# Kernel optimization log

Measured on AMD Instinct MI355X. Metric: run time of the kernel, lower is better.

## Reference

```python
import jax, jax.numpy as jnp
import numpy as np

EPS = 1e-6

def oneplus(x):
    return 1.0 + jnp.log1p(jnp.exp(x) + EPS)

def content_addr(mem, keys, strength):
    # mem [B,N,M], keys [B,R,M], strength [B,R] -> [B,R,N]
    mn = jnp.sqrt(jnp.sum(mem * mem, -1))    # [B,N]
    kn = jnp.sqrt(jnp.sum(keys * keys, -1))  # [B,R]
    sim = jnp.einsum('brm,bnm->brn', keys, mem) / (kn[..., None] * mn[:, None, :] + EPS)
    return jax.nn.softmax(strength[..., None] * sim, axis=-1)

def setup_inputs() -> dict:
    key = jax.random.key(0)
    ks = jax.random.split(key, 16)
    B, T, W, R, N, M = 16, 32, 128, 4, 512, 128
    def lin(k, fi, fo):
        k1, k2 = jax.random.split(k)
        s = 1.0 / np.sqrt(fi)
        return (jax.random.uniform(k1, (fi, fo), minval=-s, maxval=s),
                jax.random.uniform(k2, (fo,), minval=-s, maxval=s))
    Din = W + R * W  # controller input: cat(x_t, prev_reads)
    Wb, bb = lin(ks[0], Din + W, W)     # CfC backbone (1 layer, silu)
    Wff1, bff1 = lin(ks[1], W, W)
    Wff2, bff2 = lin(ks[2], W, W)
    Wta, bta = lin(ks[3], W, W)
    Wtb, btb = lin(ks[4], W, W)
    Wv, bv = lin(ks[5], W, W)
    Wr, br = lin(ks[6], W * R, W)
    Wxi, bxi = lin(ks[7], W, W * R + 3 * W + 5 * R + 3)
    X = jax.random.normal(ks[8], (B, T, W), dtype=jnp.float32)
    hs = jnp.zeros((B, W), dtype=jnp.float32)
    mem = jax.random.normal(ks[9], (B, N, M), dtype=jnp.float32) * 0.1
    reset_idxs = jax.random.randint(ks[10], (B, T), 0, 2, dtype=jnp.int32)
    return {'X': X, 'hs': hs, 'mem': mem, 'reset_idxs': reset_idxs,
            'Wb': Wb, 'bb': bb, 'Wff1': Wff1, 'bff1': bff1, 'Wff2': Wff2, 'bff2': bff2,
            'Wta': Wta, 'bta': bta, 'Wtb': Wtb, 'btb': btb,
            'Wv': Wv, 'bv': bv, 'Wr': Wr, 'br': br, 'Wxi': Wxi, 'bxi': bxi}

def dnc_forward(X, hs, mem, reset_idxs, Wb, bb, Wff1, bff1, Wff2, bff2,
                Wta, bta, Wtb, btb, Wv, bv, Wr, br, Wxi, bxi):
    B, T, W = X.shape
    N, M = mem.shape[1], mem.shape[2]
    R = (bxi.shape[0] - 3 * W - 3) // (W + 5)
    eye = jnp.eye(N, dtype=mem.dtype)

    def step(carry, inp):
        hs, memv, prev_reads, prev_rw, prev_ww, usage, prec, link = carry
        x_t, reset, t = inp
        r = reset.astype(x_t.dtype)
        memv = memv * (1 - r)[:, None, None]   # memory.reset_idx
        hs = hs * (1 - r)[:, None]
        # CfC controller cell
        z = jax.nn.silu(jnp.concatenate([x_t, prev_reads, hs], -1) @ Wb + bb)
        ff1 = z @ Wff1 + bff1
        ff2 = z @ Wff2 + bff2
        ti = jax.nn.sigmoid((z @ Wta + bta) * t + (z @ Wtb + btb))
        hs = ff1 * (1 - ti) + ti * ff2
        # interface vector split
        xi = hs @ Wxi + bxi
        p = 0
        read_keys = xi[:, :W * R].reshape(B, R, W); p = W * R
        write_key = xi[:, p:p + W]; p += W
        write_vec = xi[:, p:p + W]; p += W
        erase = jax.nn.sigmoid(xi[:, p:p + W]); p += W
        free_g = jax.nn.sigmoid(xi[:, p:p + R]); p += R
        read_str = oneplus(xi[:, p:p + R]); p += R
        read_modes = jax.nn.softmax(xi[:, p:p + 3 * R].reshape(B, R, 3), -1); p += 3 * R
        write_str = oneplus(xi[:, p:p + 1]); p += 1
        alloc_g = jax.nn.sigmoid(xi[:, p:p + 1]); p += 1
        write_g = jax.nn.sigmoid(xi[:, p:p + 1])
        # write weights
        wca = content_addr(memv, write_key[:, None, :], write_str)[:, 0]  # [B,N]
        retention = jnp.prod(1 - free_g[:, :, None] * prev_rw, axis=1)
        usage = (usage + prev_ww - usage * prev_ww) * retention
        si = jnp.argsort(usage, -1)
        cp = jnp.cumprod(jnp.take_along_axis(usage, si, -1), -1)
        alloc = (1 - usage) * jnp.take_along_axis(cp, si, -1)  # gather(1, sorted_idx), as in source
        ww = write_g * (alloc_g * alloc + (1 - alloc_g) * wca)  # [B,N]
        wc = ww[:, :, None]
        link = (1 - wc - jnp.swapaxes(wc, 1, 2)) * link + wc * prec[:, None, :]
        link = link * (1 - eye)
        prec = (1 - ww.sum(-1, keepdims=True)) * prec + ww
        memv = memv * (1 - wc * erase[:, None, :]) + wc * write_vec[:, None, :]
        # read
        rca = content_addr(memv, read_keys, read_str)              # [B,R,N]
        fw = jnp.einsum('brn,bnk->brk', prev_rw, link)
        bw = jnp.einsum('brn,bkn->brk', prev_rw, link)
        aux = jnp.stack([bw, rca, fw], 2)                          # [B,R,3,N]
        rw = (aux * read_modes[..., None]).sum(2)
        reads = jnp.einsum('brn,bnm->brm', rw, memv).reshape(B, R * M)
        y = hs @ Wv + bv + reads @ Wr + br
        # prev_reads is detached each step in the source
        carry = (hs, memv, jax.lax.stop_gradient(reads), rw, ww, usage, prec, link)
        return carry, (y, hs)

    dt = X.dtype
    init = (hs, mem,
            jnp.zeros((B, R * W), dt), jnp.zeros((B, R, N), dt), jnp.zeros((B, N), dt),
            jnp.zeros((B, N), dt), jnp.zeros((B, N), dt), jnp.zeros((B, N, N), dt))
    xs = (jnp.swapaxes(X, 0, 1), jnp.swapaxes(reset_idxs, 0, 1), jnp.arange(T, dtype=dt))
    _, (ys, hss) = jax.lax.scan(step, init, xs)
    return jnp.swapaxes(ys, 0, 1), jnp.swapaxes(hss, 0, 1)

def reference(X, hs, mem, reset_idxs, Wb, bb, Wff1, bff1, Wff2, bff2,
              Wta, bta, Wtb, btb, Wv, bv, Wr, br, Wxi, bxi):
    return dnc_forward(X, hs, mem, reset_idxs, Wb, bb, Wff1, bff1, Wff2, bff2,
                       Wta, bta, Wtb, btb, Wv, bv, Wr, br, Wxi, bxi)
```

## Files before the change

kernel.cpp:

```cpp
#include <hip/hip_runtime.h>
#include <math.h>

#define Bq 16
#define Tq 32
#define Wq 128
#define Rq 4
#define Nq 512
#define Mq 128
#define DINq 768
#define XIDq 919
#define BTWq (Bq*Tq*Wq)

#define TSTRIDE 31232
#define TF_FW    0
#define TF_BW    16384
#define TF_RCA   18432
#define TF_RW    20480
#define TF_PR    22528
#define TF_WC    26624
#define TF_WW    27136
#define TF_PREC  27648
#define TF_XI    28672
#define TF_CNT   29696

struct P {
  const float *X, *hs0, *mem0;
  const int *rst;
  const float *Wb,*bb,*Wff1,*bff1,*Wff2,*bff2,*Wta,*bta,*Wtb,*btb,*Wv,*bv,*Wr,*br,*Wxi,*bxi;
  float *out;
  float *rdh,*teams;
  float *WbT,*Wff1T,*Wff2T,*WtaT,*WtbT,*WvT,*WrT,*WxiT;
};

__device__ __forceinline__ float dot4(float4 a, float4 b){
  return a.x*b.x + a.y*b.y + a.z*b.z + a.w*b.w;
}
__device__ __forceinline__ float sigf(float x){ return 1.f/(1.f+expf(-x)); }
__device__ __forceinline__ float oneplusf(float x){ return 1.f + log1pf(expf(x) + 1e-6f); }

__device__ __forceinline__ void pst(float* p, float v){
  __hip_atomic_store(p, v, __ATOMIC_RELAXED, __HIP_MEMORY_SCOPE_AGENT);
}
__device__ __forceinline__ float pld(float* p){
  return __hip_atomic_load(p, __ATOMIC_RELAXED, __HIP_MEMORY_SCOPE_AGENT);
}
__device__ __forceinline__ void bump(unsigned* f){
  __syncthreads();
  if (threadIdx.x==0)
    __hip_atomic_fetch_add(f, 1u, __ATOMIC_RELAXED, __HIP_MEMORY_SCOPE_AGENT);
}
__device__ __forceinline__ void waitge(unsigned* f, unsigned v){
  if (threadIdx.x==0){
    while (__hip_atomic_fetch_add(f, 0u, __ATOMIC_RELAXED, __HIP_MEMORY_SCOPE_AGENT) < v)
      __builtin_amdgcn_s_sleep(1);
  }
  __syncthreads();
}

__device__ __forceinline__ float wave_sum64(float v){
  #pragma unroll
  for (int m=32;m>=1;m>>=1) v += __shfl_xor(v, m, 64);
  return v;
}
__device__ __forceinline__ float wave_max64(float v){
  #pragma unroll
  for (int m=32;m>=1;m>>=1) v = fmaxf(v, __shfl_xor(v, m, 64));
  return v;
}
__device__ __forceinline__ float blk_sum(float v, float* s8){
  int w = threadIdx.x>>6;
  v = wave_sum64(v);
  if ((threadIdx.x&63)==0) s8[w] = v;
  __syncthreads();
  float r = s8[0]+s8[1]+s8[2]+s8[3]+s8[4]+s8[5]+s8[6]+s8[7];
  __syncthreads();
  return r;
}
__device__ __forceinline__ float blk_max(float v, float* s8){
  int w = threadIdx.x>>6;
  v = wave_max64(v);
  if ((threadIdx.x&63)==0) s8[w] = v;
  __syncthreads();
  float r = s8[0];
  #pragma unroll
  for (int q=1;q<8;q++) r = fmaxf(r, s8[q]);
  __syncthreads();
  return r;
}

__global__ __launch_bounds__(256) void k_init(P p){
  int bid=blockIdx.x, tid=threadIdx.x;
  if (bid<8){ int idx=bid*256+tid, st=8*256;
    for (int k=idx;k<DINq*Wq;k+=st){ int j=k/DINq,i=k%DINq; p.WbT[k]=p.Wb[i*Wq+j]; }
  } else if (bid<10){ int idx=(bid-8)*256+tid, st=2*256;
    for (int k=idx;k<Wq*Wq;k+=st){ int j=k/Wq,i=k%Wq; p.Wff1T[k]=p.Wff1[i*Wq+j]; }
  } else if (bid<12){ int idx=(bid-10)*256+tid, st=2*256;
    for (int k=idx;k<Wq*Wq;k+=st){ int j=k/Wq,i=k%Wq; p.Wff2T[k]=p.Wff2[i*Wq+j]; }
  } else if (bid<14){ int idx=(bid-12)*256+tid, st=2*256;
    for (int k=idx;k<Wq*Wq;k+=st){ int j=k/Wq,i=k%Wq; p.WtaT[k]=p.Wta[i*Wq+j]; }
  } else if (bid<16){ int idx=(bid-14)*256+tid, st=2*256;
    for (int k=idx;k<Wq*Wq;k+=st){ int j=k/Wq,i=k%Wq; p.WtbT[k]=p.Wtb[i*Wq+j]; }
  } else if (bid<18){ int idx=(bid-16)*256+tid, st=2*256;
    for (int k=idx;k<Wq*Wq;k+=st){ int j=k/Wq,i=k%Wq; p.WvT[k]=p.Wv[i*Wq+j]; }
  } else if (bid<22){ int idx=(bid-18)*256+tid, st=4*256;
    for (int k=idx;k<Rq*Wq*Wq;k+=st){ int j=k/(Rq*Wq),i=k%(Rq*Wq); p.WrT[k]=p.Wr[i*Wq+j]; }
  } else if (bid<30){ int idx=(bid-22)*256+tid, st=8*256;
    for (int k=idx;k<XIDq*Wq;k+=st){ int f=k/Wq,i=k%Wq; p.WxiT[k]=p.Wxi[i*XIDq+f]; }
  } else if (bid<38){ int idx=(bid-30)*256+tid, st=8*256;
    for (int k=idx;k<16*TSTRIDE;k+=st) p.teams[k]=0.f;
  }
}

__global__ __launch_bounds__(512,2) void k_run(P p){
  const int tid=threadIdx.x, bid=blockIdx.x;
  const bool isA = (bid<16);
  const int team = isA ? bid : ((bid-16)>>3);
  const int g    = isA ? 0   : ((bid-16)&7);
  const int b=team;
  const int w=tid>>6, l=tid&63;
  float* T = p.teams + (size_t)team*TSTRIDE;
  unsigned* C = (unsigned*)(T+TF_CNT);
  unsigned* CNT_FW=C+0; unsigned* FLAG_RW=C+32; unsigned* CNT_RD=C+64;
  unsigned* FLAG_XI=C+96; unsigned* CNT_WC=C+128; unsigned* FLAG_WW=C+160;

  __shared__ __align__(16) float rwl[Rq*Nq];
  __shared__ __align__(16) float xil[XIDq+9];
  __shared__ __align__(16) float wwl[Nq];
  __shared__ __align__(16) float precl[Nq];
  __shared__ __align__(16) float usage[Nq];
  __shared__ __align__(16) float uarr[Nq];
  __shared__ __align__(16) float cpl[Nq];
  __shared__ __align__(16) int   sidx[Nq];
  __shared__ __align__(16) float wcas[Nq];
  __shared__ __align__(16) float inv[DINq];
  __shared__ __align__(16) float zl[Wq];
  __shared__ __align__(16) float hsl[Wq];
  __shared__ __align__(16) float acc4[4*Wq];
  __shared__ __align__(16) float scrA[Rq*Nq];
  __shared__ __align__(16) float scrB[Rq*Nq];
  __shared__ __align__(16) float scrC[Rq*Nq];
  __shared__ float s8[8];

  if (isA){
    for (int i=tid;i<Rq*Nq;i+=512) rwl[i]=0.f;
    usage[tid]=0.f; precl[tid]=0.f; wwl[tid]=0.f;
    if (tid<Wq) hsl[tid]=p.hs0[b*Wq+tid];
    __syncthreads();

    for (int t=0;t<=Tq;t++){
      if (t>0){
        waitge(CNT_FW, 8u*(unsigned)t);
        float* rcl=scrA; float* fwl=scrB; float* bwl=scrC;
        #pragma unroll
        for (int k=0;k<4;k++){
          int idx=tid+k*512;
          float f=0.f;
          #pragma unroll
          for (int gg=0;gg<8;gg++) f+=pld(T+TF_FW+gg*2048+idx);
          fwl[idx]=f;
          bwl[idx]=pld(T+TF_BW+idx);
          rcl[idx]=pld(T+TF_RCA+idx);
        }
        __syncthreads();
        #pragma unroll
        for (int r=0;r<Rq;r++){
          float v=rcl[r*Nq+tid];
          float mx=blk_max(v,s8);
          float e=expf(v-mx);
          float se=blk_sum(e,s8);
          rcl[r*Nq+tid]=e/se;
        }
        __syncthreads();
        #pragma unroll
        for (int k=0;k<4;k++){
          int idx=tid+k*512, r=idx>>9;
          float m0=xil[904+r*3],m1=xil[905+r*3],m2=xil[906+r*3];
          float mm=fmaxf(m0,fmaxf(m1,m2));
          float e0=expf(m0-mm),e1=expf(m1-mm),e2=expf(m2-mm);
          float es=e0+e1+e2;
          float rwv=(e0*bwl[idx]+e1*rcl[idx]+e2*fwl[idx])/es;
          rwl[idx]=rwv;
          pst(T+TF_RW+idx,rwv);
        }
      } else {
        #pragma unroll
        for (int k=0;k<4;k++){ int idx=tid+k*512; rwl[idx]=0.f; pst(T+TF_RW+idx,0.f); }
      }
      bump(FLAG_RW);
      waitge(CNT_RD, 8u*(unsigned)(t+1));
      if (t>0){
        float s=0.f;
        #pragma unroll
        for (int gg=0;gg<8;gg++) s+=pld(T+TF_PR+gg*512+tid);
        inv[Wq+tid]=s;
        p.rdh[((size_t)b*Tq+(t-1))*Nq+tid]=s;
      } else inv[Wq+tid]=0.f;
      if (t==Tq) break;
      __syncthreads();
      float keep=1.f-(float)p.rst[b*Tq+t];
      if (tid<Wq){ inv[tid]=p.X[((size_t)b*Tq+t)*Wq+tid]; inv[Wq+Nq+tid]=keep*hsl[tid]; }
      __syncthreads();
      { int j=tid>>2,q=tid&3;
        const float4* w4=(const float4*)(p.WbT+(size_t)j*DINq);
        const float4* i4=(const float4*)inv;
        float a=0.f;
        for (int c=q;c<192;c+=4) a+=dot4(w4[c],i4[c]);
        a+=__shfl_xor(a,1,4); a+=__shfl_xor(a,2,4);
        if (q==0){ a+=p.bb[j]; zl[j]=a*sigf(a); }
      }
      __syncthreads();
      { int which=tid>>7,j=tid&127;
        const float* Wg=(which==0)?p.Wff1T:(which==1)?p.Wff2T:(which==2)?p.WtaT:p.WtbT;
        const float4* w4=(const float4*)(Wg+(size_t)j*Wq);
        const float4* z4=(const float4*)zl;
        float a=0.f;
        #pragma unroll 8
        for (int c=0;c<32;c++) a+=dot4(w4[c],z4[c]);
        acc4[which*Wq+j]=a;
      }
      __syncthreads();
      if (tid<Wq){
        float a1=acc4[tid]+p.bff1[tid],a2=acc4[Wq+tid]+p.bff2[tid];
        float aa=acc4[2*Wq+tid]+p.bta[tid],ab=acc4[3*Wq+tid]+p.btb[tid];
        float ti=sigf(aa*(float)t+ab);
        float h=a1*(1.f-ti)+ti*a2;
        hsl[tid]=h;
        p.out[BTWq+((size_t)b*Tq+t)*Wq+tid]=h;
      }
      __syncthreads();
      { const float4* h4=(const float4*)hsl;
        { const float4* w4=(const float4*)(p.WxiT+(size_t)tid*Wq);
          float a=p.bxi[tid];
          #pragma unroll 8
          for (int c=0;c<32;c++) a+=dot4(w4[c],h4[c]);
          xil[tid]=a; pst(T+TF_XI+tid,a);
        }
        int f2=tid+512;
        if (f2<XIDq){
          const float4* w4=(const float4*)(p.WxiT+(size_t)f2*Wq);
          float a=p.bxi[f2];
          #pragma unroll 8
          for (int c=0;c<32;c++) a+=dot4(w4[c],h4[c]);
          xil[f2]=a; pst(T+TF_XI+f2,a);
        }
      }
      bump(FLAG_XI);
      int n=tid;
      float ret=1.f;
      #pragma unroll
      for (int r=0;r<Rq;r++) ret*=1.f-sigf(xil[896+r])*rwl[r*Nq+n];
      float uo=usage[n],pw=wwl[n];
      float u=(uo+pw-uo*pw)*ret;
      usage[n]=u; uarr[n]=u;
      __syncthreads();
      int rank=0;
      const float4* u4=(const float4*)uarr;
      #pragma unroll 8
      for (int jj=0;jj<128;jj++){
        float4 vv=u4[jj]; int j0=jj*4;
        rank+=(vv.x<u)||(vv.x==u&&(j0+0)<n);
        rank+=(vv.y<u)||(vv.y==u&&(j0+1)<n);
        rank+=(vv.z<u)||(vv.z==u&&(j0+2)<n);
        rank+=(vv.w<u)||(vv.w==u&&(j0+3)<n);
      }
      sidx[rank]=n;
      __syncthreads();
      int si=sidx[n];
      float sv=uarr[si];
      float x=sv;
      #pragma unroll
      for (int dd=1;dd<64;dd<<=1){ float pr=__shfl_up(x,dd,64); if (l>=dd) x*=pr; }
      if (l==63) s8[w]=x;
      __syncthreads();
      float woff=1.f;
      #pragma unroll
      for (int q=0;q<8;q++) if (q<w) woff*=s8[q];
      x*=woff;
      cpl[n]=x;
      waitge(CNT_WC, 8u*(unsigned)(t+1));
      { float v=pld(T+TF_WC+tid);
        float mx=blk_max(v,s8);
        float e=expf(v-mx);
        float se=blk_sum(e,s8);
        wcas[tid]=e/se;
      }
      __syncthreads();
      float alloc=(1.f-u)*cpl[si];
      float ag=sigf(xil[917]),wg=sigf(xil[918]);
      float wwv=wg*(ag*alloc+(1.f-ag)*wcas[n]);
      wwl[n]=wwv;
      pst(T+TF_WW+n,wwv);
      float wsum=blk_sum(wwv,s8);
      float pn=(1.f-wsum)*precl[n]+wwv;
      precl[n]=pn;
      pst(T+TF_PREC+(t&1)*Nq+n,pn);
      bump(FLAG_WW);
    }
  } else {
    const int rg=l>>3, cg=l&7;
    const int n_own=g*64+w*8+rg;
    const int c0=cg*16;
    float4 m4[4]; float nrm;
    { const float4* src=(const float4*)(p.mem0+((size_t)b*Nq+n_own)*Mq+c0);
      float s=0.f;
      #pragma unroll
      for (int i=0;i<4;i++){ m4[i]=src[i]; s+=dot4(m4[i],m4[i]); }
      s+=__shfl_xor(s,1,8); s+=__shfl_xor(s,2,8); s+=__shfl_xor(s,4,8);
      nrm=sqrtf(s);
    }
    float Lreg[8][8];
    #pragma unroll
    for (int rr=0;rr<8;rr++)
      #pragma unroll
      for (int q=0;q<8;q++) Lreg[rr][q]=0.f;

    for (int t=0;t<=Tq;t++){
      waitge(FLAG_RW, (unsigned)(t+1));
      for (int i=tid;i<Rq*Nq;i+=512) rwl[i]=pld(T+TF_RW+i);
      float* prl=wcas;
      prl[tid]=0.f;
      __syncthreads();
      #pragma unroll
      for (int r=0;r<Rq;r++){
        float rwn=rwl[r*Nq+n_own];
        #pragma unroll
        for (int i=0;i<4;i++){
          float ax=rwn*m4[i].x, ay=rwn*m4[i].y, az=rwn*m4[i].z, aw=rwn*m4[i].w;
          ax+=__shfl_xor(ax,8,64); ax+=__shfl_xor(ax,16,64); ax+=__shfl_xor(ax,32,64);
          ay+=__shfl_xor(ay,8,64); ay+=__shfl_xor(ay,16,64); ay+=__shfl_xor(ay,32,64);
          az+=__shfl_xor(az,8,64); az+=__shfl_xor(az,16,64); az+=__shfl_xor(az,32,64);
          aw+=__shfl_xor(aw,8,64); aw+=__shfl_xor(aw,16,64); aw+=__shfl_xor(aw,32,64);
          if (rg==0){
            atomicAdd(&prl[r*Wq+c0+i*4+0],ax);
            atomicAdd(&prl[r*Wq+c0+i*4+1],ay);
            atomicAdd(&prl[r*Wq+c0+i*4+2],az);
            atomicAdd(&prl[r*Wq+c0+i*4+3],aw);
          }
        }
      }
      __syncthreads();
      pst(T+TF_PR+g*512+tid, prl[tid]);
      bump(CNT_RD);
      if (t==Tq) break;
      waitge(FLAG_XI, (unsigned)(t+1));
      { xil[tid]=pld(T+TF_XI+tid);
        int f2=tid+512; if (f2<XIDq) xil[f2]=pld(T+TF_XI+f2); }
      __syncthreads();
      float keep=1.f-(float)p.rst[b*Tq+t];
      { float kk=(tid<Wq)? xil[512+tid]*xil[512+tid]:0.f;
        float kn=sqrtf(blk_sum(kk,s8));
        const float4* k4=(const float4*)(xil+512);
        float d=0.f;
        #pragma unroll
        for (int i=0;i<4;i++) d+=dot4(k4[cg*4+i],m4[i]);
        d+=__shfl_xor(d,1,8); d+=__shfl_xor(d,2,8); d+=__shfl_xor(d,4,8);
        float wstr=oneplusf(xil[916]);
        float sim=(keep*d)/(kn*(keep*nrm)+1e-6f);
        if (cg==0) pst(T+TF_WC+n_own, wstr*sim);
      }
      bump(CNT_WC);
      precl[tid]=pld(T+TF_PREC+((t&1)^1)*Nq+tid);
      waitge(FLAG_WW,(unsigned)(t+1));
      wwl[tid]=pld(T+TF_WW+tid);
      __syncthreads();
      { float* fwacc=scrA;
        int c0p=l*8;
        float ww8[8],pc8[8],pr8[Rq][8];
        *(float4*)&ww8[0]=*(const float4*)&wwl[c0p];   *(float4*)&ww8[4]=*(const float4*)&wwl[c0p+4];
        *(float4*)&pc8[0]=*(const float4*)&precl[c0p]; *(float4*)&pc8[4]=*(const float4*)&precl[c0p+4];
        #pragma unroll
        for (int r=0;r<Rq;r++){
          *(float4*)&pr8[r][0]=*(const float4*)&rwl[r*Nq+c0p];
          *(float4*)&pr8[r][4]=*(const float4*)&rwl[r*Nq+c0p+4];
        }
        float fa[Rq][8];
        #pragma unroll
        for (int r=0;r<Rq;r++)
          #pragma unroll
          for (int q=0;q<8;q++) fa[r][q]=0.f;
        #pragma unroll
        for (int rr=0;rr<8;rr++){
          int n2=g*64+w*8+rr;
          float wwn=wwl[n2];
          float prn[Rq];
          #pragma unroll
          for (int r=0;r<Rq;r++) prn[r]=rwl[r*Nq+n2];
          float bwp[Rq]={0.f,0.f,0.f,0.f};
          #pragma unroll
          for (int q=0;q<8;q++){
            float nv=(1.f-wwn-ww8[q])*Lreg[rr][q]+wwn*pc8[q];
            if (c0p+q==n2) nv=0.f;
            Lreg[rr][q]=nv;
            #pragma unroll
            for (int r=0;r<Rq;r++){ fa[r][q]+=prn[r]*nv; bwp[r]+=pr8[r][q]*nv; }
          }
          #pragma unroll
          for (int mm=1;mm<64;mm<<=1)
            #pragma unroll
            for (int r=0;r<Rq;r++) bwp[r]+=__shfl_xor(bwp[r],mm,64);
          if (l==0){
            #pragma unroll
            for (int r=0;r<Rq;r++) pst(T+TF_BW+r*Nq+n2, bwp[r]);
          }
        }
        for (int k=0;k<8;k++){
          if (w==k){
            #pragma unroll
            for (int r=0;r<Rq;r++)
              #pragma unroll
              for (int q=0;q<8;q++){
                if (k==0) fwacc[r*Nq+c0p+q]=fa[r][q];
                else      fwacc[r*Nq+c0p+q]+=fa[r][q];
              }
          }
          __syncthreads();
        }
        for (int i=tid;i<Rq*Nq;i+=512) pst(T+TF_FW+g*2048+i,fwacc[i]);
      }
      { float wwn=wwl[n_own];
        float s=0.f;
        #pragma unroll
        for (int i=0;i<4;i++){
          float e0=sigf(xil[768+c0+i*4+0]), e1=sigf(xil[768+c0+i*4+1]);
          float e2=sigf(xil[768+c0+i*4+2]), e3=sigf(xil[768+c0+i*4+3]);
          m4[i].x = m4[i].x*keep*(1.f-wwn*e0) + wwn*xil[640+c0+i*4+0];
          m4[i].y = m4[i].y*keep*(1.f-wwn*e1) + wwn*xil[640+c0+i*4+1];
          m4[i].z = m4[i].z*keep*(1.f-wwn*e2) + wwn*xil[640+c0+i*4+2];
          m4[i].w = m4[i].w*keep*(1.f-wwn*e3) + wwn*xil[640+c0+i*4+3];
          s+=dot4(m4[i],m4[i]);
        }
        s+=__shfl_xor(s,1,8); s+=__shfl_xor(s,2,8); s+=__shfl_xor(s,4,8);
        nrm=sqrtf(s);
        float kn4[Rq], rstr[Rq];
        #pragma unroll
        for (int r=0;r<Rq;r++){
          float kk=(tid<Wq)? xil[r*Wq+tid]*xil[r*Wq+tid]:0.f;
          kn4[r]=sqrtf(blk_sum(kk,s8));
          rstr[r]=oneplusf(xil[900+r]);
        }
        #pragma unroll
        for (int r=0;r<Rq;r++){
          const float4* kr=(const float4*)(xil+r*Wq);
          float d=0.f;
          #pragma unroll
          for (int i=0;i<4;i++) d+=dot4(kr[cg*4+i],m4[i]);
          d+=__shfl_xor(d,1,8); d+=__shfl_xor(d,2,8); d+=__shfl_xor(d,4,8);
          float v=rstr[r]*(d/(kn4[r]*nrm+1e-6f));
          if (cg==0) pst(T+TF_RCA+r*Nq+n_own, v);
        }
      }
      bump(CNT_FW);
    }
  }
}

__global__ __launch_bounds__(512) void k_y(P p){
  int j=blockIdx.x, tid=threadIdx.x;
  __shared__ __align__(16) float wv[Wq];
  __shared__ __align__(16) float wr[Rq*Wq];
  if (tid<Wq) wv[tid]=p.WvT[(size_t)j*Wq+tid];
  wr[tid]=p.WrT[(size_t)j*(Rq*Wq)+tid];
  __syncthreads();
  int b=tid>>5, t=tid&31;
  const float4* h4=(const float4*)(p.out+BTWq+((size_t)b*Tq+t)*Wq);
  const float4* r4=(const float4*)(p.rdh+((size_t)b*Tq+t)*Nq);
  const float4* wv4=(const float4*)wv;
  const float4* wr4=(const float4*)wr;
  float a=0.f;
  #pragma unroll 8
  for (int c=0;c<32;c++) a+=dot4(wv4[c],h4[c]);
  #pragma unroll 8
  for (int c=0;c<128;c++) a+=dot4(wr4[c],r4[c]);
  p.out[((size_t)b*Tq+t)*Wq+j]=a+p.bv[j]+p.br[j];
}

extern "C" void kernel_launch(void* const* d_in, const int* in_sizes, int n_in,
                              void* d_out, int out_size, void* d_ws, size_t ws_size,
                              hipStream_t stream){
  (void)in_sizes; (void)n_in; (void)out_size; (void)ws_size;
  P p;
  p.X    = (const float*)d_in[0];
  p.hs0  = (const float*)d_in[1];
  p.mem0 = (const float*)d_in[2];
  p.rst  = (const int*)d_in[3];
  p.Wb   = (const float*)d_in[4];  p.bb   = (const float*)d_in[5];
  p.Wff1 = (const float*)d_in[6];  p.bff1 = (const float*)d_in[7];
  p.Wff2 = (const float*)d_in[8];  p.bff2 = (const float*)d_in[9];
  p.Wta  = (const float*)d_in[10]; p.bta  = (const float*)d_in[11];
  p.Wtb  = (const float*)d_in[12]; p.btb  = (const float*)d_in[13];
  p.Wv   = (const float*)d_in[14]; p.bv   = (const float*)d_in[15];
  p.Wr   = (const float*)d_in[16]; p.br   = (const float*)d_in[17];
  p.Wxi  = (const float*)d_in[18]; p.bxi  = (const float*)d_in[19];
  p.out  = (float*)d_out;
  float* ws = (float*)d_ws;
  size_t o = 0;
  p.rdh   = ws + o; o += (size_t)Bq*Tq*Nq;
  p.teams = ws + o; o += (size_t)16*TSTRIDE;
  p.WbT   = ws + o; o += (size_t)DINq*Wq;
  p.Wff1T = ws + o; o += (size_t)Wq*Wq;
  p.Wff2T = ws + o; o += (size_t)Wq*Wq;
  p.WtaT  = ws + o; o += (size_t)Wq*Wq;
  p.WtbT  = ws + o; o += (size_t)Wq*Wq;
  p.WvT   = ws + o; o += (size_t)Wq*Wq;
  p.WrT   = ws + o; o += (size_t)Rq*Wq*Wq;
  p.WxiT  = ws + o; o += (size_t)XIDq*Wq;

  hipLaunchKernelGGL(k_init, dim3(38),  dim3(256), 0, stream, p);
  hipLaunchKernelGGL(k_run,  dim3(144), dim3(512), 0, stream, p);
  hipLaunchKernelGGL(k_y,    dim3(128), dim3(512), 0, stream, p);
}
```

Measured before the change: 2.567 ms.

## Move memory matrix into controller block registers to cut cross-block handoffs

After: 2.722 ms. 6.0% more time.

```diff
diff --git a/kernel.cpp b/kernel.cpp
--- a/kernel.cpp
+++ b/kernel.cpp
@@ -11,17 +11,13 @@
 #define XIDq 919
 #define BTWq (Bq*Tq*Wq)
 
-#define TSTRIDE 31232
+#define TSTRIDE 22272
 #define TF_FW    0
 #define TF_BW    16384
-#define TF_RCA   18432
-#define TF_RW    20480
-#define TF_PR    22528
-#define TF_WC    26624
-#define TF_WW    27136
-#define TF_PREC  27648
-#define TF_XI    28672
-#define TF_CNT   29696
+#define TF_RW    18432
+#define TF_WW    20480
+#define TF_PREC  20992
+#define TF_CNT   22016
 
 struct P {
   const float *X, *hs0, *mem0;
@@ -51,7 +47,7 @@
 }
 __device__ __forceinline__ void waitge(unsigned* f, unsigned v){
   if (threadIdx.x==0){
-    while (__hip_atomic_fetch_add(f, 0u, __ATOMIC_RELAXED, __HIP_MEMORY_SCOPE_AGENT) < v)
+    while (__hip_atomic_load(f, __ATOMIC_RELAXED, __HIP_MEMORY_SCOPE_AGENT) < v)
       __builtin_amdgcn_s_sleep(1);
   }
   __syncthreads();
@@ -86,6 +82,18 @@
   for (int q=1;q<8;q++) r = fmaxf(r, s8[q]);
   __syncthreads();
   return r;
+}
+__device__ __forceinline__ float red_rg(float v){
+  v += __shfl_xor(v, 8, 64);
+  v += __shfl_xor(v, 16, 64);
+  v += __shfl_xor(v, 32, 64);
+  return v;
+}
+__device__ __forceinline__ float red_cg(float v){
+  v += __shfl_xor(v, 1, 8);
+  v += __shfl_xor(v, 2, 8);
+  v += __shfl_xor(v, 4, 8);
+  return v;
 }
 
 __global__ __launch_bounds__(256) void k_init(P p){
@@ -111,19 +119,22 @@
   }
 }
 
-__global__ __launch_bounds__(512,2) void k_run(P p){
+__global__ __launch_bounds__(512,1) void k_run(P p){
   const int tid=threadIdx.x, bid=blockIdx.x;
   const bool isA = (bid<16);
   const int team = isA ? bid : ((bid-16)>>3);
   const int g    = isA ? 0   : ((bid-16)&7);
   const int b=team;
   const int w=tid>>6, l=tid&63;
+  const int rg=l>>3, cg=l&7, c0=cg*16;
   float* T = p.teams + (size_t)team*TSTRIDE;
   unsigned* C = (unsigned*)(T+TF_CNT);
-  unsigned* CNT_FW=C+0; unsigned* FLAG_RW=C+32; unsigned* CNT_RD=C+64;
-  unsigned* FLAG_XI=C+96; unsigned* CNT_WC=C+128; unsigned* FLAG_WW=C+160;
+  unsigned* CNT_FW=C+0; unsigned* FLAG_RW=C+32; unsigned* FLAG_WW=C+64;
 
   __shared__ __align__(16) float rwl[Rq*Nq];
+  __shared__ __align__(16) float rcl[Rq*Nq];
+  __shared__ __align__(16) float fwl[Rq*Nq];
+  __shared__ __align__(16) float bwl[Rq*Nq];
   __shared__ __align__(16) float xil[XIDq+9];
   __shared__ __align__(16) float wwl[Nq];
   __shared__ __align__(16) float precl[Nq];
@@ -136,12 +147,19 @@
   __shared__ __align__(16) float zl[Wq];
   __shared__ __align__(16) float hsl[Wq];
   __shared__ __align__(16) float acc4[4*Wq];
-  __shared__ __align__(16) float scrA[Rq*Nq];
-  __shared__ __align__(16) float scrB[Rq*Nq];
-  __shared__ __align__(16) float scrC[Rq*Nq];
   __shared__ float s8[8];
 
   if (isA){
+    float4 m4[8][4];
+    float  nrm[8];
+    #pragma unroll
+    for (int g2=0;g2<8;g2++){
+      const float4* src=(const float4*)(p.mem0 + ((size_t)b*Nq + g2*64 + w*8 + rg)*Mq + c0);
+      float s=0.f;
+      #pragma unroll
+      for (int i=0;i<4;i++){ m4[g2][i]=src[i]; s+=dot4(m4[g2][i],m4[g2][i]); }
+      nrm[g2]=sqrtf(red_cg(s));
+    }
     for (int i=tid;i<Rq*Nq;i+=512) rwl[i]=0.f;
     usage[tid]=0.f; precl[tid]=0.f; wwl[tid]=0.f;
     if (tid<Wq) hsl[tid]=p.hs0[b*Wq+tid];
@@ -150,7 +168,6 @@
     for (int t=0;t<=Tq;t++){
       if (t>0){
         waitge(CNT_FW, 8u*(unsigned)t);
-        float* rcl=scrA; float* fwl=scrB; float* bwl=scrC;
         #pragma unroll
         for (int k=0;k<4;k++){
           int idx=tid+k*512;
@@ -159,7 +176,6 @@
           for (int gg=0;gg<8;gg++) f+=pld(T+TF_FW+gg*2048+idx);
           fwl[idx]=f;
           bwl[idx]=pld(T+TF_BW+idx);
-          rcl[idx]=pld(T+TF_RCA+idx);
         }
         __syncthreads();
         #pragma unroll
@@ -187,16 +203,43 @@
         for (int k=0;k<4;k++){ int idx=tid+k*512; rwl[idx]=0.f; pst(T+TF_RW+idx,0.f); }
       }
       bump(FLAG_RW);
-      waitge(CNT_RD, 8u*(unsigned)(t+1));
-      if (t>0){
-        float s=0.f;
-        #pragma unroll
-        for (int gg=0;gg<8;gg++) s+=pld(T+TF_PR+gg*512+tid);
-        inv[Wq+tid]=s;
-        p.rdh[((size_t)b*Tq+(t-1))*Nq+tid]=s;
-      } else inv[Wq+tid]=0.f;
+      { float* prl=wcas;
+        prl[tid]=0.f;
+        __syncthreads();
+        if (t>0){
+          #pragma unroll
+          for (int r=0;r<Rq;r++){
+            float4 a0=make_float4(0.f,0.f,0.f,0.f),a1=a0,a2=a0,a3=a0;
+            #pragma unroll
+            for (int g2=0;g2<8;g2++){
+              float rwn=rwl[r*Nq + g2*64 + w*8 + rg];
+              a0.x+=rwn*m4[g2][0].x; a0.y+=rwn*m4[g2][0].y; a0.z+=rwn*m4[g2][0].z; a0.w+=rwn*m4[g2][0].w;
+              a1.x+=rwn*m4[g2][1].x; a1.y+=rwn*m4[g2][1].y; a1.z+=rwn*m4[g2][1].z; a1.w+=rwn*m4[g2][1].w;
+              a2.x+=rwn*m4[g2][2].x; a2.y+=rwn*m4[g2][2].y; a2.z+=rwn*m4[g2][2].z; a2.w+=rwn*m4[g2][2].w;
+              a3.x+=rwn*m4[g2][3].x; a3.y+=rwn*m4[g2][3].y; a3.z+=rwn*m4[g2][3].z; a3.w+=rwn*m4[g2][3].w;
+            }
+            a0.x=red_rg(a0.x); a0.y=red_rg(a0.y); a0.z=red_rg(a0.z); a0.w=red_rg(a0.w);
+            a1.x=red_rg(a1.x); a1.y=red_rg(a1.y); a1.z=red_rg(a1.z); a1.w=red_rg(a1.w);
+            a2.x=red_rg(a2.x); a2.y=red_rg(a2.y); a2.z=red_rg(a2.z); a2.w=red_rg(a2.w);
+            a3.x=red_rg(a3.x); a3.y=red_rg(a3.y); a3.z=red_rg(a3.z); a3.w=red_rg(a3.w);
+            if (rg==0){
+              atomicAdd(&prl[r*Wq+c0+ 0],a0.x); atomicAdd(&prl[r*Wq+c0+ 1],a0.y);
+              atomicAdd(&prl[r*Wq+c0+ 2],a0.z); atomicAdd(&prl[r*Wq+c0+ 3],a0.w);
+              atomicAdd(&prl[r*Wq+c0+ 4],a1.x); atomicAdd(&prl[r*Wq+c0+ 5],a1.y);
+              atomicAdd(&prl[r*Wq+c0+ 6],a1.z); atomicAdd(&prl[r*Wq+c0+ 7],a1.w);
+              atomicAdd(&prl[r*Wq+c0+ 8],a2.x); atomicAdd(&prl[r*Wq+c0+ 9],a2.y);
+              atomicAdd(&prl[r*Wq+c0+10],a2.z); atomicAdd(&prl[r*Wq+c0+11],a2.w);
+              atomicAdd(&prl[r*Wq+c0+12],a3.x); atomicAdd(&prl[r*Wq+c0+13],a3.y);
+              atomicAdd(&prl[r*Wq+c0+14],a3.z); atomicAdd(&prl[r*Wq+c0+15],a3.w);
+            }
+          }
+        }
+        __syncthreads();
+        inv[Wq+tid]=prl[tid];
+        if (t>0) p.rdh[((size_t)b*Tq+(t-1))*Nq+tid]=prl[tid];
+        __syncthreads();
+      }
       if (t==Tq) break;
-      __syncthreads();
       float keep=1.f-(float)p.rst[b*Tq+t];
       if (tid<Wq){ inv[tid]=p.X[((size_t)b*Tq+t)*Wq+tid]; inv[Wq+Nq+tid]=keep*hsl[tid]; }
       __syncthreads();
@@ -233,7 +276,7 @@
           float a=p.bxi[tid];
           #pragma unroll 8
           for (int c=0;c<32;c++) a+=dot4(w4[c],h4[c]);
-          xil[tid]=a; pst(T+TF_XI+tid,a);
+          xil[tid]=a;
         }
         int f2=tid+512;
         if (f2<XIDq){
@@ -241,129 +284,133 @@
           float a=p.bxi[f2];
           #pragma unroll 8
           for (int c=0;c<32;c++) a+=dot4(w4[c],h4[c]);
-          xil[f2]=a; pst(T+TF_XI+f2,a);
-        }
-      }
-      bump(FLAG_XI);
-      int n=tid;
-      float ret=1.f;
-      #pragma unroll
-      for (int r=0;r<Rq;r++) ret*=1.f-sigf(xil[896+r])*rwl[r*Nq+n];
-      float uo=usage[n],pw=wwl[n];
-      float u=(uo+pw-uo*pw)*ret;
-      usage[n]=u; uarr[n]=u;
-      __syncthreads();
-      int rank=0;
-      const float4* u4=(const float4*)uarr;
-      #pragma unroll 8
-      for (int jj=0;jj<128;jj++){
-        float4 vv=u4[jj]; int j0=jj*4;
-        rank+=(vv.x<u)||(vv.x==u&&(j0+0)<n);
-        rank+=(vv.y<u)||(vv.y==u&&(j0+1)<n);
-        rank+=(vv.z<u)||(vv.z==u&&(j0+2)<n);
-        rank+=(vv.w<u)||(vv.w==u&&(j0+3)<n);
-      }
-      sidx[rank]=n;
-      __syncthreads();
-      int si=sidx[n];
-      float sv=uarr[si];
-      float x=sv;
-      #pragma unroll
-      for (int dd=1;dd<64;dd<<=1){ float pr=__shfl_up(x,dd,64); if (l>=dd) x*=pr; }
-      if (l==63) s8[w]=x;
-      __syncthreads();
-      float woff=1.f;
-      #pragma unroll
-      for (int q=0;q<8;q++) if (q<w) woff*=s8[q];
-      x*=woff;
-      cpl[n]=x;
-      waitge(CNT_WC, 8u*(unsigned)(t+1));
-      { float v=pld(T+TF_WC+tid);
+          xil[f2]=a;
+        }
+      }
+      __syncthreads();
+      { float kk=(tid<Wq)? xil[512+tid]*xil[512+tid]:0.f;
+        float kn=sqrtf(blk_sum(kk,s8));
+        const float4* k4=(const float4*)(xil+512);
+        float wstr=oneplusf(xil[916]);
+        #pragma unroll
+        for (int g2=0;g2<8;g2++){
+          float d=dot4(k4[cg*4+0],m4[g2][0])+dot4(k4[cg*4+1],m4[g2][1])
+                 +dot4(k4[cg*4+2],m4[g2][2])+dot4(k4[cg*4+3],m4[g2][3]);
+          d=red_cg(d);
+          float sim=(keep*d)/(kn*(keep*nrm[g2])+1e-6f);
+          if (cg==0) wcas[g2*64+w*8+rg]=wstr*sim;
+        }
+        __syncthreads();
+        float v=wcas[tid];
         float mx=blk_max(v,s8);
         float e=expf(v-mx);
         float se=blk_sum(e,s8);
         wcas[tid]=e/se;
       }
       __syncthreads();
-      float alloc=(1.f-u)*cpl[si];
-      float ag=sigf(xil[917]),wg=sigf(xil[918]);
-      float wwv=wg*(ag*alloc+(1.f-ag)*wcas[n]);
-      wwl[n]=wwv;
-      pst(T+TF_WW+n,wwv);
-      float wsum=blk_sum(wwv,s8);
-      float pn=(1.f-wsum)*precl[n]+wwv;
-      precl[n]=pn;
-      pst(T+TF_PREC+(t&1)*Nq+n,pn);
+      { int n=tid;
+        float ret=1.f;
+        #pragma unroll
+        for (int r=0;r<Rq;r++) ret*=1.f-sigf(xil[896+r])*rwl[r*Nq+n];
+        float uo=usage[n],pw=wwl[n];
+        float u=(uo+pw-uo*pw)*ret;
+        usage[n]=u; uarr[n]=u;
+        __syncthreads();
+        int rank=0;
+        const float4* u4=(const float4*)uarr;
+        #pragma unroll 8
+        for (int jj=0;jj<128;jj++){
+          float4 vv=u4[jj]; int j0=jj*4;
+          rank+=(vv.x<u)||(vv.x==u&&(j0+0)<n);
+          rank+=(vv.y<u)||(vv.y==u&&(j0+1)<n);
+          rank+=(vv.z<u)||(vv.z==u&&(j0+2)<n);
+          rank+=(vv.w<u)||(vv.w==u&&(j0+3)<n);
+        }
+        sidx[rank]=n;
+        __syncthreads();
+        int si=sidx[n];
+        float sv=uarr[si];
+        float x=sv;
+        #pragma unroll
+        for (int dd=1;dd<64;dd<<=1){ float pr=__shfl_up(x,dd,64); if (l>=dd) x*=pr; }
+        if (l==63) s8[w]=x;
+        __syncthreads();
+        float woff=1.f;
+        #pragma unroll
+        for (int q=0;q<8;q++) if (q<w) woff*=s8[q];
+        x*=woff;
+        cpl[n]=x;
+        __syncthreads();
+        float alloc=(1.f-u)*cpl[si];
+        float ag=sigf(xil[917]),wg=sigf(xil[918]);
+        float wwv=wg*(ag*alloc+(1.f-ag)*wcas[n]);
+        wwl[n]=wwv;
+        pst(T+TF_WW+n,wwv);
+        float wsum=blk_sum(wwv,s8);
+        float pn=(1.f-wsum)*precl[n]+wwv;
+        precl[n]=pn;
+        pst(T+TF_PREC+(t&1)*Nq+n,pn);
+      }
       bump(FLAG_WW);
+      { float4 e4v[4], wv4v[4];
+        #pragma unroll
+        for (int i=0;i<4;i++){
+          e4v[i].x=sigf(xil[768+c0+i*4+0]); e4v[i].y=sigf(xil[768+c0+i*4+1]);
+          e4v[i].z=sigf(xil[768+c0+i*4+2]); e4v[i].w=sigf(xil[768+c0+i*4+3]);
+          wv4v[i].x=xil[640+c0+i*4+0]; wv4v[i].y=xil[640+c0+i*4+1];
+          wv4v[i].z=xil[640+c0+i*4+2]; wv4v[i].w=xil[640+c0+i*4+3];
+        }
+        #pragma unroll
+        for (int g2=0;g2<8;g2++){
+          float wwn=wwl[g2*64+w*8+rg];
+          float s=0.f;
+          #pragma unroll
+          for (int i=0;i<4;i++){
+            m4[g2][i].x=m4[g2][i].x*keep*(1.f-wwn*e4v[i].x)+wwn*wv4v[i].x;
+            m4[g2][i].y=m4[g2][i].y*keep*(1.f-wwn*e4v[i].y)+wwn*wv4v[i].y;
+            m4[g2][i].z=m4[g2][i].z*keep*(1.f-wwn*e4v[i].z)+wwn*wv4v[i].z;
+            m4[g2][i].w=m4[g2][i].w*keep*(1.f-wwn*e4v[i].w)+wwn*wv4v[i].w;
+            s+=dot4(m4[g2][i],m4[g2][i]);
+          }
+          nrm[g2]=sqrtf(red_cg(s));
+        }
+        float kn4[Rq], rstr[Rq];
+        #pragma unroll
+        for (int r=0;r<Rq;r++){
+          float kk=(tid<Wq)? xil[r*Wq+tid]*xil[r*Wq+tid]:0.f;
+          kn4[r]=sqrtf(blk_sum(kk,s8));
+          rstr[r]=oneplusf(xil[900+r]);
+        }
+        #pragma unroll
+        for (int r=0;r<Rq;r++){
+          const float4* kr=(const float4*)(xil+r*Wq);
+          #pragma unroll
+          for (int g2=0;g2<8;g2++){
+            float d=dot4(kr[cg*4+0],m4[g2][0])+dot4(kr[cg*4+1],m4[g2][1])
+                   +dot4(kr[cg*4+2],m4[g2][2])+dot4(kr[cg*4+3],m4[g2][3]);
+            d=red_cg(d);
+            float v=rstr[r]*(d/(kn4[r]*nrm[g2]+1e-6f));
+            if (cg==0) rcl[r*Nq+g2*64+w*8+rg]=v;
+          }
+        }
+      }
+      __syncthreads();
     }
   } else {
-    const int rg=l>>3, cg=l&7;
-    const int n_own=g*64+w*8+rg;
-    const int c0=cg*16;
-    float4 m4[4]; float nrm;
-    { const float4* src=(const float4*)(p.mem0+((size_t)b*Nq+n_own)*Mq+c0);
-      float s=0.f;
-      #pragma unroll
-      for (int i=0;i<4;i++){ m4[i]=src[i]; s+=dot4(m4[i],m4[i]); }
-      s+=__shfl_xor(s,1,8); s+=__shfl_xor(s,2,8); s+=__shfl_xor(s,4,8);
-      nrm=sqrtf(s);
-    }
     float Lreg[8][8];
     #pragma unroll
     for (int rr=0;rr<8;rr++)
       #pragma unroll
       for (int q=0;q<8;q++) Lreg[rr][q]=0.f;
 
-    for (int t=0;t<=Tq;t++){
+    for (int t=0;t<Tq;t++){
       waitge(FLAG_RW, (unsigned)(t+1));
       for (int i=tid;i<Rq*Nq;i+=512) rwl[i]=pld(T+TF_RW+i);
-      float* prl=wcas;
-      prl[tid]=0.f;
-      __syncthreads();
-      #pragma unroll
-      for (int r=0;r<Rq;r++){
-        float rwn=rwl[r*Nq+n_own];
-        #pragma unroll
-        for (int i=0;i<4;i++){
-          float ax=rwn*m4[i].x, ay=rwn*m4[i].y, az=rwn*m4[i].z, aw=rwn*m4[i].w;
-          ax+=__shfl_xor(ax,8,64); ax+=__shfl_xor(ax,16,64); ax+=__shfl_xor(ax,32,64);
-          ay+=__shfl_xor(ay,8,64); ay+=__shfl_xor(ay,16,64); ay+=__shfl_xor(ay,32,64);
-          az+=__shfl_xor(az,8,64); az+=__shfl_xor(az,16,64); az+=__shfl_xor(az,32,64);
-          aw+=__shfl_xor(aw,8,64); aw+=__shfl_xor(aw,16,64); aw+=__shfl_xor(aw,32,64);
-          if (rg==0){
-            atomicAdd(&prl[r*Wq+c0+i*4+0],ax);
-            atomicAdd(&prl[r*Wq+c0+i*4+1],ay);
-            atomicAdd(&prl[r*Wq+c0+i*4+2],az);
-            atomicAdd(&prl[r*Wq+c0+i*4+3],aw);
-          }
-        }
-      }
-      __syncthreads();
-      pst(T+TF_PR+g*512+tid, prl[tid]);
-      bump(CNT_RD);
-      if (t==Tq) break;
-      waitge(FLAG_XI, (unsigned)(t+1));
-      { xil[tid]=pld(T+TF_XI+tid);
-        int f2=tid+512; if (f2<XIDq) xil[f2]=pld(T+TF_XI+f2); }
-      __syncthreads();
-      float keep=1.f-(float)p.rst[b*Tq+t];
-      { float kk=(tid<Wq)? xil[512+tid]*xil[512+tid]:0.f;
-        float kn=sqrtf(blk_sum(kk,s8));
-        const float4* k4=(const float4*)(xil+512);
-        float d=0.f;
-        #pragma unroll
-        for (int i=0;i<4;i++) d+=dot4(k4[cg*4+i],m4[i]);
-        d+=__shfl_xor(d,1,8); d+=__shfl_xor(d,2,8); d+=__shfl_xor(d,4,8);
-        float wstr=oneplusf(xil[916]);
-        float sim=(keep*d)/(kn*(keep*nrm)+1e-6f);
-        if (cg==0) pst(T+TF_WC+n_own, wstr*sim);
-      }
-      bump(CNT_WC);
       precl[tid]=pld(T+TF_PREC+((t&1)^1)*Nq+tid);
       waitge(FLAG_WW,(unsigned)(t+1));
       wwl[tid]=pld(T+TF_WW+tid);
       __syncthreads();
-      { float* fwacc=scrA;
+      { float* fwacc=fwl;
         int c0p=l*8;
         float ww8[8],pc8[8],pr8[Rq][8];
         *(float4*)&ww8[0]=*(const float4*)&wwl[c0p];   *(float4*)&ww8[4]=*(const float4*)&wwl[c0p+4];
@@ -416,38 +463,6 @@
           __syncthreads();
         }
         for (int i=tid;i<Rq*Nq;i+=512) pst(T+TF_FW+g*2048+i,fwacc[i]);
-      }
-      { float wwn=wwl[n_own];
-        float s=0.f;
-        #pragma unroll
-        for (int i=0;i<4;i++){
-          float e0=sigf(xil[768+c0+i*4+0]), e1=sigf(xil[768+c0+i*4+1]);
-          float e2=sigf(xil[768+c0+i*4+2]), e3=sigf(xil[768+c0+i*4+3]);
-          m4[i].x = m4[i].x*keep*(1.f-wwn*e0) + wwn*xil[640+c0+i*4+0];
-          m4[i].y = m4[i].y*keep*(1.f-wwn*e1) + wwn*xil[640+c0+i*4+1];
-          m4[i].z = m4[i].z*keep*(1.f-wwn*e2) + wwn*xil[640+c0+i*4+2];
-          m4[i].w = m4[i].w*keep*(1.f-wwn*e3) + wwn*xil[640+c0+i*4+3];
-          s+=dot4(m4[i],m4[i]);
-        }
-        s+=__shfl_xor(s,1,8); s+=__shfl_xor(s,2,8); s+=__shfl_xor(s,4,8);
-        nrm=sqrtf(s);
-        float kn4[Rq], rstr[Rq];
-        #pragma unroll
-        for (int r=0;r<Rq;r++){
-          float kk=(tid<Wq)? xil[r*Wq+tid]*xil[r*Wq+tid]:0.f;
-          kn4[r]=sqrtf(blk_sum(kk,s8));
-          rstr[r]=oneplusf(xil[900+r]);
-        }
-        #pragma unroll
-        for (int r=0;r<Rq;r++){
-          const float4* kr=(const float4*)(xil+r*Wq);
-          float d=0.f;
-          #pragma unroll
-          for (int i=0;i<4;i++) d+=dot4(kr[cg*4+i],m4[i]);
-          d+=__shfl_xor(d,1,8); d+=__shfl_xor(d,2,8); d+=__shfl_xor(d,4,8);
-          float v=rstr[r]*(d/(kn4[r]*nrm+1e-6f));
-          if (cg==0) pst(T+TF_RCA+r*Nq+n_own, v);
-        }
       }
       bump(CNT_FW);
     }
```

## Use volatile cross-block exchange when validated, and prefetch input part of backbone matvec

Applied to the files above, without the earlier changes.

Result: slower. 3.142 ms (+22.4%).

```diff
diff --git a/kernel.cpp b/kernel.cpp
--- a/kernel.cpp
+++ b/kernel.cpp
@@ -11,7 +11,7 @@
 #define XIDq 919
 #define BTWq (Bq*Tq*Wq)
 
-#define TSTRIDE 31232
+#define TSTRIDE 30720
 #define TF_FW    0
 #define TF_BW    16384
 #define TF_RCA   18432
@@ -21,7 +21,8 @@
 #define TF_WW    27136
 #define TF_PREC  27648
 #define TF_XI    28672
-#define TF_CNT   29696
+#define TF_MAGIC 29696
+#define TF_CNT   30208
 
 struct P {
   const float *X, *hs0, *mem0;
@@ -44,6 +45,12 @@
 __device__ __forceinline__ float pld(float* p){
   return __hip_atomic_load(p, __ATOMIC_RELAXED, __HIP_MEMORY_SCOPE_AGENT);
 }
+__device__ __forceinline__ void PSTf(float* p, float v, bool fast){
+  if (fast) *(volatile float*)p = v; else pst(p, v);
+}
+__device__ __forceinline__ float PLDf(float* p, bool fast){
+  return fast ? *(volatile const float*)p : pld(p);
+}
 __device__ __forceinline__ void bump(unsigned* f){
   __syncthreads();
   if (threadIdx.x==0)
@@ -51,7 +58,7 @@
 }
 __device__ __forceinline__ void waitge(unsigned* f, unsigned v){
   if (threadIdx.x==0){
-    while (__hip_atomic_fetch_add(f, 0u, __ATOMIC_RELAXED, __HIP_MEMORY_SCOPE_AGENT) < v)
+    while (__hip_atomic_load(f, __ATOMIC_RELAXED, __HIP_MEMORY_SCOPE_AGENT) < v)
       __builtin_amdgcn_s_sleep(1);
   }
   __syncthreads();
@@ -86,6 +93,12 @@
   for (int q=1;q<8;q++) r = fmaxf(r, s8[q]);
   __syncthreads();
   return r;
+}
+__device__ __forceinline__ float red_cg(float v){
+  v += __shfl_xor(v, 1, 8);
+  v += __shfl_xor(v, 2, 8);
+  v += __shfl_xor(v, 4, 8);
+  return v;
 }
 
 __global__ __launch_bounds__(256) void k_init(P p){
@@ -106,7 +119,7 @@
     for (int k=idx;k<Rq*Wq*Wq;k+=st){ int j=k/(Rq*Wq),i=k%(Rq*Wq); p.WrT[k]=p.Wr[i*Wq+j]; }
   } else if (bid<30){ int idx=(bid-22)*256+tid, st=8*256;
     for (int k=idx;k<XIDq*Wq;k+=st){ int f=k/Wq,i=k%Wq; p.WxiT[k]=p.Wxi[i*XIDq+f]; }
-  } else if (bid<38){ int idx=(bid-30)*256+tid, st=8*256;
+  } else if (bid<40){ int idx=(bid-30)*256+tid, st=10*256;
     for (int k=idx;k<16*TSTRIDE;k+=st) p.teams[k]=0.f;
   }
 }
@@ -114,14 +127,15 @@
 __global__ __launch_bounds__(512,2) void k_run(P p){
   const int tid=threadIdx.x, bid=blockIdx.x;
   const bool isA = (bid<16);
-  const int team = isA ? bid : ((bid-16)>>3);
-  const int g    = isA ? 0   : ((bid-16)&7);
+  const int team = isA ? bid : ((bid-16)&15);
+  const int g    = isA ? 0   : ((bid-16)>>4);
   const int b=team;
   const int w=tid>>6, l=tid&63;
   float* T = p.teams + (size_t)team*TSTRIDE;
   unsigned* C = (unsigned*)(T+TF_CNT);
   unsigned* CNT_FW=C+0; unsigned* FLAG_RW=C+32; unsigned* CNT_RD=C+64;
   unsigned* FLAG_XI=C+96; unsigned* CNT_WC=C+128; unsigned* FLAG_WW=C+160;
+  unsigned* VFLAG=C+192; unsigned* CNT_V=C+224; unsigned* OKF=C+240;
 
   __shared__ __align__(16) float rwl[Rq*Nq];
   __shared__ __align__(16) float xil[XIDq+9];
@@ -141,6 +155,22 @@
   __shared__ __align__(16) float scrC[Rq*Nq];
   __shared__ float s8[8];
 
+  bool fast;
+  if (isA){
+    if (tid==0) __hip_atomic_store(OKF, 1u, __ATOMIC_RELAXED, __HIP_MEMORY_SCOPE_AGENT);
+    *(volatile float*)(T+TF_MAGIC+tid) = (float)(tid*3+7);
+    bump(VFLAG);
+    waitge(CNT_V, 8u);
+  } else {
+    waitge(VFLAG, 1u);
+    bool ok = (*(volatile const float*)(T+TF_MAGIC+tid) == (float)(tid*3+7));
+    if (!ok) __hip_atomic_fetch_and(OKF, 0u, __ATOMIC_RELAXED, __HIP_MEMORY_SCOPE_AGENT);
+    bump(CNT_V);
+    waitge(CNT_V, 8u);
+  }
+  fast = (__hip_atomic_load(OKF, __ATOMIC_RELAXED, __HIP_MEMORY_SCOPE_AGENT) != 0u);
+  __syncthreads();
+
   if (isA){
     for (int i=tid;i<Rq*Nq;i+=512) rwl[i]=0.f;
     usage[tid]=0.f; precl[tid]=0.f; wwl[tid]=0.f;
@@ -148,6 +178,22 @@
     __syncthreads();
 
     for (int t=0;t<=Tq;t++){
+      float keep=0.f;
+      if (t<Tq){
+        keep=1.f-(float)p.rst[b*Tq+t];
+        if (tid<Wq){ inv[tid]=p.X[((size_t)b*Tq+t)*Wq+tid]; inv[Wq+Nq+tid]=keep*hsl[tid]; }
+        __syncthreads();
+        int j=tid>>2,q=tid&3;
+        const float4* w4=(const float4*)(p.WbT+(size_t)j*DINq);
+        const float4* i4=(const float4*)inv;
+        float a=0.f;
+        #pragma unroll
+        for (int c=q;c<32;c+=4) a+=dot4(w4[c],i4[c]);
+        #pragma unroll
+        for (int c=160+q;c<192;c+=4) a+=dot4(w4[c],i4[c]);
+        a+=__shfl_xor(a,1,4); a+=__shfl_xor(a,2,4);
+        if (q==0) zl[j]=a+p.bb[j];
+      }
       if (t>0){
         waitge(CNT_FW, 8u*(unsigned)t);
         float* rcl=scrA; float* fwl=scrB; float* bwl=scrC;
@@ -156,10 +202,10 @@
           int idx=tid+k*512;
           float f=0.f;
           #pragma unroll
-          for (int gg=0;gg<8;gg++) f+=pld(T+TF_FW+gg*2048+idx);
+          for (int gg=0;gg<8;gg++) f+=PLDf(T+TF_FW+gg*2048+idx,fast);
           fwl[idx]=f;
-          bwl[idx]=pld(T+TF_BW+idx);
-          rcl[idx]=pld(T+TF_RCA+idx);
+          bwl[idx]=PLDf(T+TF_BW+idx,fast);
+          rcl[idx]=PLDf(T+TF_RCA+idx,fast);
         }
         __syncthreads();
         #pragma unroll
@@ -180,33 +226,30 @@
           float es=e0+e1+e2;
           float rwv=(e0*bwl[idx]+e1*rcl[idx]+e2*fwl[idx])/es;
           rwl[idx]=rwv;
-          pst(T+TF_RW+idx,rwv);
+          PSTf(T+TF_RW+idx,rwv,fast);
         }
       } else {
         #pragma unroll
-        for (int k=0;k<4;k++){ int idx=tid+k*512; rwl[idx]=0.f; pst(T+TF_RW+idx,0.f); }
+        for (int k=0;k<4;k++){ int idx=tid+k*512; rwl[idx]=0.f; PSTf(T+TF_RW+idx,0.f,fast); }
       }
       bump(FLAG_RW);
       waitge(CNT_RD, 8u*(unsigned)(t+1));
       if (t>0){
         float s=0.f;
         #pragma unroll
-        for (int gg=0;gg<8;gg++) s+=pld(T+TF_PR+gg*512+tid);
+        for (int gg=0;gg<8;gg++) s+=PLDf(T+TF_PR+gg*512+tid,fast);
         inv[Wq+tid]=s;
         p.rdh[((size_t)b*Tq+(t-1))*Nq+tid]=s;
       } else inv[Wq+tid]=0.f;
       if (t==Tq) break;
       __syncthreads();
-      float keep=1.f-(float)p.rst[b*Tq+t];
-      if (tid<Wq){ inv[tid]=p.X[((size_t)b*Tq+t)*Wq+tid]; inv[Wq+Nq+tid]=keep*hsl[tid]; }
-      __syncthreads();
       { int j=tid>>2,q=tid&3;
         const float4* w4=(const float4*)(p.WbT+(size_t)j*DINq);
         const float4* i4=(const float4*)inv;
         float a=0.f;
-        for (int c=q;c<192;c+=4) a+=dot4(w4[c],i4[c]);
+        for (int c=32+q;c<160;c+=4) a+=dot4(w4[c],i4[c]);
         a+=__shfl_xor(a,1,4); a+=__shfl_xor(a,2,4);
-        if (q==0){ a+=p.bb[j]; zl[j]=a*sigf(a); }
+        if (q==0){ float z=zl[j]+a; zl[j]=z*sigf(z); }
       }
       __syncthreads();
       { int which=tid>>7,j=tid&127;
@@ -233,7 +276,7 @@
           float a=p.bxi[tid];
           #pragma unroll 8
           for (int c=0;c<32;c++) a+=dot4(w4[c],h4[c]);
-          xil[tid]=a; pst(T+TF_XI+tid,a);
+          xil[tid]=a; PSTf(T+TF_XI+tid,a,fast);
         }
         int f2=tid+512;
         if (f2<XIDq){
@@ -241,7 +284,7 @@
           float a=p.bxi[f2];
           #pragma unroll 8
           for (int c=0;c<32;c++) a+=dot4(w4[c],h4[c]);
-          xil[f2]=a; pst(T+TF_XI+f2,a);
+          xil[f2]=a; PSTf(T+TF_XI+f2,a,fast);
         }
       }
       bump(FLAG_XI);
@@ -278,7 +321,7 @@
       x*=woff;
       cpl[n]=x;
       waitge(CNT_WC, 8u*(unsigned)(t+1));
-      { float v=pld(T+TF_WC+tid);
+      { float v=PLDf(T+TF_WC+tid,fast);
         float mx=blk_max(v,s8);
         float e=expf(v-mx);
         float se=blk_sum(e,s8);
@@ -289,11 +332,11 @@
       float ag=sigf(xil[917]),wg=sigf(xil[918]);
       float wwv=wg*(ag*alloc+(1.f-ag)*wcas[n]);
       wwl[n]=wwv;
-      pst(T+TF_WW+n,wwv);
+      PSTf(T+TF_WW+n,wwv,fast);
       float wsum=blk_sum(wwv,s8);
       float pn=(1.f-wsum)*precl[n]+wwv;
       precl[n]=pn;
-      pst(T+TF_PREC+(t&1)*Nq+n,pn);
+      PSTf(T+TF_PREC+(t&1)*Nq+n,pn,fast);
       bump(FLAG_WW);
     }
   } else {
@@ -305,8 +348,7 @@
       float s=0.f;
       #pragma unroll
       for (int i=0;i<4;i++){ m4[i]=src[i]; s+=dot4(m4[i],m4[i]); }
-      s+=__shfl_xor(s,1,8); s+=__shfl_xor(s,2,8); s+=__shfl_xor(s,4,8);
-      nrm=sqrtf(s);
+      nrm=sqrtf(red_cg(s));
     }
     float Lreg[8][8];
     #pragma unroll
@@ -316,7 +358,7 @@
 
     for (int t=0;t<=Tq;t++){
       waitge(FLAG_RW, (unsigned)(t+1));
-      for (int i=tid;i<Rq*Nq;i+=512) rwl[i]=pld(T+TF_RW+i);
+      for (int i=tid;i<Rq*Nq;i+=512) rwl[i]=PLDf(T+TF_RW+i,fast);
       float* prl=wcas;
       prl[tid]=0.f;
       __syncthreads();
@@ -339,12 +381,12 @@
         }
       }
       __syncthreads();
-      pst(T+TF_PR+g*512+tid, prl[tid]);
+      PSTf(T+TF_PR+g*512+tid, prl[tid],fast);
       bump(CNT_RD);
       if (t==Tq) break;
       waitge(FLAG_XI, (unsigned)(t+1));
-      { xil[tid]=pld(T+TF_XI+tid);
-        int f2=tid+512; if (f2<XIDq) xil[f2]=pld(T+TF_XI+f2); }
+      { xil[tid]=PLDf(T+TF_XI+tid,fast);
+        int f2=tid+512; if (f2<XIDq) xil[f2]=PLDf(T+TF_XI+f2,fast); }
       __syncthreads();
       float keep=1.f-(float)p.rst[b*Tq+t];
       { float kk=(tid<Wq)? xil[512+tid]*xil[512+tid]:0.f;
@@ -353,15 +395,15 @@
         float d=0.f;
         #pragma unroll
         for (int i=0;i<4;i++) d+=dot4(k4[cg*4+i],m4[i]);
-        d+=__shfl_xor(d,1,8); d+=__shfl_xor(d,2,8); d+=__shfl_xor(d,4,8);
+        d=red_cg(d);
         float wstr=oneplusf(xil[916]);
         float sim=(keep*d)/(kn*(keep*nrm)+1e-6f);
-        if (cg==0) pst(T+TF_WC+n_own, wstr*sim);
+        if (cg==0) PSTf(T+TF_WC+n_own, wstr*sim,fast);
       }
       bump(CNT_WC);
-      precl[tid]=pld(T+TF_PREC+((t&1)^1)*Nq+tid);
+      precl[tid]=PLDf(T+TF_PREC+((t&1)^1)*Nq+tid,fast);
       waitge(FLAG_WW,(unsigned)(t+1));
-      wwl[tid]=pld(T+TF_WW+tid);
+      wwl[tid]=PLDf(T+TF_WW+tid,fast);
       __syncthreads();
       { float* fwacc=scrA;
         int c0p=l*8;
@@ -400,7 +442,7 @@
             for (int r=0;r<Rq;r++) bwp[r]+=__shfl_xor(bwp[r],mm,64);
           if (l==0){
             #pragma unroll
-            for (int r=0;r<Rq;r++) pst(T+TF_BW+r*Nq+n2, bwp[r]);
+            for (int r=0;r<Rq;r++) PSTf(T+TF_BW+r*Nq+n2, bwp[r],fast);
           }
         }
         for (int k=0;k<8;k++){
@@ -415,7 +457,7 @@
           }
           __syncthreads();
         }
-        for (int i=tid;i<Rq*Nq;i+=512) pst(T+TF_FW+g*2048+i,fwacc[i]);
+        for (int i=tid;i<Rq*Nq;i+=512) PSTf(T+TF_FW+g*2048+i,fwacc[i],fast);
       }
       { float wwn=wwl[n_own];
         float s=0.f;
@@ -423,14 +465,13 @@
         for (int i=0;i<4;i++){
           float e0=sigf(xil[768+c0+i*4+0]), e1=sigf(xil[768+c0+i*4+1]);
           float e2=sigf(xil[768+c0+i*4+2]), e3=sigf(xil[768+c0+i*4+3]);
-          m4[i].x = m4[i].x*keep*(1.f-wwn*e0) + wwn*xil[640+c0+i*4+0];
-          m4[i].y = m4[i].y*keep*(1.f-wwn*e1) + wwn*xil[640+c0+i*4+1];
-          m4[i].z = m4[i].z*keep*(1.f-wwn*e2) + wwn*xil[640+c0+i*4+2];
-          m4[i].w = m4[i].w*keep*(1.f-wwn*e3) + wwn*xil[640+c0+i*4+3];
+          m4[i].x=m4[i].x*keep*(1.f-wwn*e0)+wwn*xil[640+c0+i*4+0];
+          m4[i].y=m4[i].y*keep*(1.f-wwn*e1)+wwn*xil[640+c0+i*4+1];
+          m4[i].z=m4[i].z*keep*(1.f-wwn*e2)+wwn*xil[640+c0+i*4+2];
+          m4[i].w=m4[i].w*keep*(1.f-wwn*e3)+wwn*xil[640+c0+i*4+3];
           s+=dot4(m4[i],m4[i]);
         }
-        s+=__shfl_xor(s,1,8); s+=__shfl_xor(s,2,8); s+=__shfl_xor(s,4,8);
-        nrm=sqrtf(s);
+        nrm=sqrtf(red_cg(s));
         float kn4[Rq], rstr[Rq];
         #pragma unroll
         for (int r=0;r<Rq;r++){
@@ -444,9 +485,9 @@
           float d=0.f;
           #pragma unroll
           for (int i=0;i<4;i++) d+=dot4(kr[cg*4+i],m4[i]);
-          d+=__shfl_xor(d,1,8); d+=__shfl_xor(d,2,8); d+=__shfl_xor(d,4,8);
+          d=red_cg(d);
           float v=rstr[r]*(d/(kn4[r]*nrm+1e-6f));
-          if (cg==0) pst(T+TF_RCA+r*Nq+n_own, v);
+          if (cg==0) PSTf(T+TF_RCA+r*Nq+n_own, v,fast);
         }
       }
       bump(CNT_FW);
@@ -505,7 +546,7 @@
   p.WrT   = ws + o; o += (size_t)Rq*Wq*Wq;
   p.WxiT  = ws + o; o += (size_t)XIDq*Wq;
 
-  hipLaunchKernelGGL(k_init, dim3(38),  dim3(256), 0, stream, p);
+  hipLaunchKernelGGL(k_init, dim3(40),  dim3(256), 0, stream, p);
   hipLaunchKernelGGL(k_run,  dim3(144), dim3(512), 0, stream, p);
   hipLaunchKernelGGL(k_y,    dim3(128), dim3(512), 0, stream, p);
 }
```
